# Performance work log

Measured on AMD Instinct MI355X. Metric: run time of the kernel, lower is better.

## Reference

```python
import jax, jax.numpy as jnp
import numpy as np

N_LOW, N_HIGH = 20000, 60000
E_LOW, E_L2H, E_HIGH = 320000, 540000, 480000
EPS = 1e-5
NEG_SLOPE = 0.2


def _gatv2(x_src, x_dst, edge_index, Wl, Wr, att, bias):
    """PyG GATv2Conv with concat heads, aggr='mean', no self loops.
    att: [H, C]. Returns [n_dst, H*C]."""
    H, C = att.shape
    n_dst = x_dst.shape[0]
    xl = (x_src @ Wl).reshape(-1, H, C)   # [n_src, H, C]
    xr = (x_dst @ Wr).reshape(-1, H, C)   # [n_dst, H, C]
    src, dst = edge_index[0], edge_index[1]
    z = jax.nn.leaky_relu(xl[src] + xr[dst], NEG_SLOPE)        # [E, H, C]
    logits = jnp.einsum('ehc,hc->eh', z, att)                  # [E, H]
    m = jax.ops.segment_max(logits, dst, num_segments=n_dst)   # segment softmax
    e = jnp.exp(logits - m[dst])
    s = jax.ops.segment_sum(e, dst, num_segments=n_dst)
    alpha = e / s[dst]                                         # [E, H]
    out = jax.ops.segment_sum(xl[src] * alpha[:, :, None], dst, num_segments=n_dst)
    deg = jax.ops.segment_sum(jnp.ones((src.shape[0],), out.dtype), dst, num_segments=n_dst)
    out = out / jnp.maximum(deg, 1.0)[:, None, None]           # aggr='mean'
    out = out.reshape(n_dst, H * C)
    if bias is not None:
        out = out + bias
    return out


def _bn(x, g, b):
    mu = x.mean(axis=0)
    var = x.var(axis=0)
    return (x - mu) * jax.lax.rsqrt(var + EPS) * g + b


def _forward(x_low, x_high, z_std, e_low, e_l2h, e_high,
             l1_Wl, l1_Wr, l1_att, l1_b, bn1_g, bn1_b,
             l2_Wl, l2_Wr, l2_att, l2_b, bn2_g, bn2_b,
             l3_Wl, l3_Wr, l3_att, l3_b,
             lh_Wl, lh_Wr, lh_att,
             h1_Wl, h1_Wr, h1_att, h1_b, bn3_g, bn3_b,
             h2_Wl, h2_Wr, h2_att, h2_b, bn4_g, bn4_b,
             h3_Wl, h3_Wr, h3_att, h3_b):
    # low_net: GATv2(125->128,h2) -> BN(256) -> GATv2(256->128) -> BN(128) -> GATv2(128->128)
    h = _gatv2(x_low, x_low, e_low, l1_Wl, l1_Wr, l1_att, l1_b)
    h = _bn(h, bn1_g, bn1_b)
    h = _gatv2(h, h, e_low, l2_Wl, l2_Wr, l2_att, l2_b)
    h = _bn(h, bn2_g, bn2_b)
    h = _gatv2(h, h, e_low, l3_Wl, l3_Wr, l3_att, l3_b)
    # bipartite low2high: (encod_low[128], x_high[1]) -> 128, no bias
    eh = _gatv2(h, x_high, e_l2h, lh_Wl, lh_Wr, lh_att, None)
    eh = jnp.concatenate([z_std, eh], axis=-1)                 # [N_HIGH, 129]
    # high_net
    g = _gatv2(eh, eh, e_high, h1_Wl, h1_Wr, h1_att, h1_b)
    g = _bn(g, bn3_g, bn3_b)
    g = _gatv2(g, g, e_high, h2_Wl, h2_Wr, h2_att, h2_b)
    g = _bn(g, bn4_g, bn4_b)
    return _gatv2(g, g, e_high, h3_Wl, h3_Wr, h3_att, h3_b)   # [N_HIGH, 2]


def setup_inputs() -> dict:
    key = jax.random.key(0)
    ks = iter(jax.random.split(key, 64))
    def P(shape, fan_in):
        return jax.random.normal(next(ks), shape, jnp.float32) / np.sqrt(fan_in)
    inp = {}
    inp['x_low'] = jax.random.normal(next(ks), (N_LOW, 125), jnp.float32)
    inp['x_high'] = jax.random.normal(next(ks), (N_HIGH, 1), jnp.float32)
    inp['z_std'] = jax.random.normal(next(ks), (N_HIGH, 1), jnp.float32)
    inp['e_low'] = jnp.stack([jax.random.randint(next(ks), (E_LOW,), 0, N_LOW),
                              jax.random.randint(next(ks), (E_LOW,), 0, N_LOW)])
    inp['e_l2h'] = jnp.stack([jax.random.randint(next(ks), (E_L2H,), 0, N_LOW),
                              jax.random.randint(next(ks), (E_L2H,), 0, N_HIGH)])
    inp['e_high'] = jnp.stack([jax.random.randint(next(ks), (E_HIGH,), 0, N_HIGH),
                               jax.random.randint(next(ks), (E_HIGH,), 0, N_HIGH)])
    inp['l1_Wl'] = P((125, 256), 125); inp['l1_Wr'] = P((125, 256), 125)
    inp['l1_att'] = P((2, 128), 128);  inp['l1_b'] = jnp.zeros((256,), jnp.float32)
    inp['bn1_g'] = jnp.ones((256,), jnp.float32); inp['bn1_b'] = jnp.zeros((256,), jnp.float32)
    inp['l2_Wl'] = P((256, 128), 256); inp['l2_Wr'] = P((256, 128), 256)
    inp['l2_att'] = P((1, 128), 128);  inp['l2_b'] = jnp.zeros((128,), jnp.float32)
    inp['bn2_g'] = jnp.ones((128,), jnp.float32); inp['bn2_b'] = jnp.zeros((128,), jnp.float32)
    inp['l3_Wl'] = P((128, 128), 128); inp['l3_Wr'] = P((128, 128), 128)
    inp['l3_att'] = P((1, 128), 128);  inp['l3_b'] = jnp.zeros((128,), jnp.float32)
    inp['lh_Wl'] = P((128, 128), 128); inp['lh_Wr'] = P((1, 128), 1)
    inp['lh_att'] = P((1, 128), 128)
    inp['h1_Wl'] = P((129, 256), 129); inp['h1_Wr'] = P((129, 256), 129)
    inp['h1_att'] = P((2, 128), 128);  inp['h1_b'] = jnp.zeros((256,), jnp.float32)
    inp['bn3_g'] = jnp.ones((256,), jnp.float32); inp['bn3_b'] = jnp.zeros((256,), jnp.float32)
    inp['h2_Wl'] = P((256, 128), 256); inp['h2_Wr'] = P((256, 128), 256)
    inp['h2_att'] = P((1, 128), 128);  inp['h2_b'] = jnp.zeros((128,), jnp.float32)
    inp['bn4_g'] = jnp.ones((128,), jnp.float32); inp['bn4_b'] = jnp.zeros((128,), jnp.float32)
    inp['h3_Wl'] = P((128, 2), 128);   inp['h3_Wr'] = P((128, 2), 128)
    inp['h3_att'] = P((1, 2), 2);      inp['h3_b'] = jnp.zeros((2,), jnp.float32)
    return inp


def reference(x_low, x_high, z_std, e_low, e_l2h, e_high,
              l1_Wl, l1_Wr, l1_att, l1_b, bn1_g, bn1_b,
              l2_Wl, l2_Wr, l2_att, l2_b, bn2_g, bn2_b,
              l3_Wl, l3_Wr, l3_att, l3_b,
              lh_Wl, lh_Wr, lh_att,
              h1_Wl, h1_Wr, h1_att, h1_b, bn3_g, bn3_b,
              h2_Wl, h2_Wr, h2_att, h2_b, bn4_g, bn4_b,
              h3_Wl, h3_Wr, h3_att, h3_b):
    return _forward(x_low, x_high, z_std, e_low, e_l2h, e_high,
                    l1_Wl, l1_Wr, l1_att, l1_b, bn1_g, bn1_b,
                    l2_Wl, l2_Wr, l2_att, l2_b, bn2_g, bn2_b,
                    l3_Wl, l3_Wr, l3_att, l3_b,
                    lh_Wl, lh_Wr, lh_att,
                    h1_Wl, h1_Wr, h1_att, h1_b, bn3_g, bn3_b,
                    h2_Wl, h2_Wr, h2_att, h2_b, bn4_g, bn4_b,
                    h3_Wl, h3_Wr, h3_att, h3_b)
```

## Files before the change

kernel.cpp:

```cpp
#include <hip/hip_runtime.h>
#include <hip/hip_bf16.h>
#include <cstdint>
#include <cstddef>
#include <cmath>

#define NEG_SLOPE 0.2f

#define PB  1024
#define CSH 10
#define CBS 1024
#define NBCMAX 160
#define PBN 2048

using frag = __attribute__((ext_vector_type(8))) short;
using facc = __attribute__((ext_vector_type(4))) float;

__device__ __forceinline__ float bf_hi(unsigned u) {
    union { unsigned i; float f; } t; t.i = u & 0xffff0000u; return t.f;
}
__device__ __forceinline__ float bf_lo(unsigned u) {
    union { unsigned i; float f; } t; t.i = u << 16; return t.f;
}
__device__ __forceinline__ void unpack8(uint4 u, float* v) {
    v[0] = bf_lo(u.x); v[1] = bf_hi(u.x);
    v[2] = bf_lo(u.y); v[3] = bf_hi(u.y);
    v[4] = bf_lo(u.z); v[5] = bf_hi(u.z);
    v[6] = bf_lo(u.w); v[7] = bf_hi(u.w);
}

typedef const __attribute__((address_space(1))) void* gas_cptr;
typedef __attribute__((address_space(3))) void* las_ptr;
__device__ __forceinline__ void gload_lds16(const __hip_bfloat16* g, __hip_bfloat16* l) {
    __builtin_amdgcn_global_load_lds((gas_cptr)(const void*)g, (las_ptr)(void*)l, 16, 0, 0);
}

__global__ __launch_bounds__(256)
void msplitA(const int* __restrict__ s0, const int* __restrict__ d0, int E0,
             const int* __restrict__ s1, const int* __restrict__ d1, int E1,
             const int* __restrict__ s2, const int* __restrict__ d2, int E2,
             int nc0, int nc1, int nc2, int cap0, int cap1, int cap2,
             int* __restrict__ stage, int* __restrict__ cnt2) {
    __shared__ int hist[NBCMAX];
    __shared__ int rbase[NBCMAX];
    __shared__ int curs[NBCMAX];
    __shared__ int ord[1024];
    __shared__ int obkt[1024];
    const int NBC = nc0 + nc1 + nc2;
    const long Etot = (long)E0 + E1 + E2;
    int tid = threadIdx.x;
    int lane = tid & 63;
    long chunk = (Etot + PB - 1) / PB;
    long c0 = (long)blockIdx.x * chunk;
    long c1 = c0 + chunk; if (c1 > Etot) c1 = Etot;
    const long sec1 = (long)PB * nc0 * cap0;
    const long sec2 = sec1 + (long)PB * nc1 * cap1;
    for (int t = tid; t < NBC; t += 256) curs[t] = 0;
    __syncthreads();
    for (long r0 = c0; r0 < c1; r0 += 1024) {
        int n = (int)((c1 - r0 < 1024) ? (c1 - r0) : 1024);
        for (int t = tid; t < NBC; t += 256) hist[t] = 0;
        __syncthreads();
        int mye[4], myb[4], myr[4];
#pragma unroll
        for (int k = 0; k < 4; ++k) {
            int li = k * 256 + tid;
            myb[k] = -1;
            if (li < n) {
                long i = r0 + li;
                int src, dst, gb;
                if (i < E0) { src = s0[i]; dst = d0[i]; gb = dst >> CSH; }
                else if (i < (long)E0 + E1) { long j = i - E0; src = s1[j]; dst = d1[j]; gb = nc0 + (dst >> CSH); }
                else { long j = i - E0 - E1; src = s2[j]; dst = d2[j]; gb = nc0 + nc1 + (dst >> CSH); }
                mye[k] = (src << CSH) | (dst & (CBS - 1));
                myb[k] = gb;
                myr[k] = atomicAdd(&hist[gb], 1);
            }
        }
        __syncthreads();
        if (tid < 64) {
            int carry = 0;
            for (int base = 0; base < NBC; base += 64) {
                int g = base + lane;
                int v = (g < NBC) ? hist[g] : 0;
                int sum = v;
#pragma unroll
                for (int o = 1; o < 64; o <<= 1) {
                    int t = __shfl_up(sum, o, 64);
                    if (lane >= o) sum += t;
                }
                if (g < NBC) rbase[g] = carry + sum - v;
                carry += __shfl(sum, 63, 64);
            }
        }
        __syncthreads();
#pragma unroll
        for (int k = 0; k < 4; ++k)
            if (myb[k] >= 0) {
                int pos = rbase[myb[k]] + myr[k];
                ord[pos] = mye[k];
                obkt[pos] = myb[k];
            }
        __syncthreads();
        for (int pos = tid; pos < n; pos += 256) {
            int b = obkt[pos];
            int rank = pos - rbase[b] + curs[b];
            long addr; int cap;
            if (b < nc0)            { cap = cap0; addr = (long)(blockIdx.x * nc0 + b) * cap0; }
            else if (b < nc0 + nc1) { cap = cap1; addr = sec1 + (long)(blockIdx.x * nc1 + (b - nc0)) * cap1; }
            else                    { cap = cap2; addr = sec2 + (long)(blockIdx.x * nc2 + (b - nc0 - nc1)) * cap2; }
            if (rank < cap) stage[addr + rank] = ord[pos];
        }
        __syncthreads();
        for (int t = tid; t < NBC; t += 256) curs[t] += hist[t];
        __syncthreads();
    }
    for (int t = tid; t < NBC; t += 256) {
        int cap = (t < nc0) ? cap0 : (t < nc0 + nc1) ? cap1 : cap2;
        int c = curs[t]; if (c > cap) c = cap;
        cnt2[(long)blockIdx.x * NBC + t] = c;
    }
}

__global__ void scanC1(const int* __restrict__ cnt2, int* __restrict__ tot, int NBC) {
    __shared__ int red[256];
    int gb = blockIdx.x;
    int tid = threadIdx.x;
    int s = 0;
    for (int p = tid; p < PB; p += 256) s += cnt2[(long)p * NBC + gb];
    red[tid] = s;
    __syncthreads();
    for (int o = 128; o; o >>= 1) {
        if (tid < o) red[tid] += red[tid + o];
        __syncthreads();
    }
    if (tid == 0) tot[gb] = red[0];
}

__global__ void scanC2(const int* __restrict__ tot, int* __restrict__ cstart,
                       int NBC, int nc0, int nc1) {
    if (threadIdx.x == 0) {
        int c = 0;
        for (int gb = 0; gb < NBC; ++gb) {
            if (gb == nc0 || gb == nc0 + nc1) c = 0;
            cstart[gb] = c;
            c += tot[gb];
        }
    }
}

__global__ __launch_bounds__(1024)
void fineB(const int* __restrict__ cnt2, const int* __restrict__ cstart,
           const int* __restrict__ stage,
           int nc0, int nc1, int nc2, int cap0, int cap1, int cap2,
           int* __restrict__ off0, int* __restrict__ col0, int n0,
           int* __restrict__ off1, int* __restrict__ col1, int n1,
           int* __restrict__ off2, int* __restrict__ col2, int n2) {
    __shared__ int fragb[PB + 1];
    __shared__ int cnt[1024];
    __shared__ int wsum[17];
    const int NBC = nc0 + nc1 + nc2;
    int gb = blockIdx.x;
    int tid = threadIdx.x;
    int lane = tid & 63;
    int wv = tid >> 6;
    int cb, ncg, n; long base2, stride; int* off; int* col;
    const long sec1 = (long)PB * nc0 * cap0;
    const long sec2 = sec1 + (long)PB * nc1 * cap1;
    if (gb < nc0) {
        cb = gb; ncg = nc0; n = n0; off = off0; col = col0;
        base2 = (long)cb * cap0; stride = (long)nc0 * cap0;
    } else if (gb < nc0 + nc1) {
        cb = gb - nc0; ncg = nc1; n = n1; off = off1; col = col1;
        base2 = sec1 + (long)cb * cap1; stride = (long)nc1 * cap1;
    } else {
        cb = gb - nc0 - nc1; ncg = nc2; n = n2; off = off2; col = col2;
        base2 = sec2 + (long)cb * cap2; stride = (long)nc2 * cap2;
    }
    int dlo = cb << CSH;
    int colbase = cstart[gb];
    int v = cnt2[(long)tid * NBC + gb];
    int sum = v;
#pragma unroll
    for (int o = 1; o < 64; o <<= 1) {
        int t = __shfl_up(sum, o, 64);
        if (lane >= o) sum += t;
    }
    if (lane == 63) wsum[wv] = sum;
    __syncthreads();
    if (tid == 0) {
        int c = 0;
        for (int w = 0; w < 16; ++w) { int t = wsum[w]; wsum[w] = c; c += t; }
        wsum[16] = c;
    }
    __syncthreads();
    fragb[tid] = wsum[wv] + sum - v;
    if (tid == 0) fragb[PB] = wsum[16];
    __syncthreads();
    int sz = fragb[PB];
    cnt[tid] = 0;
    __syncthreads();
    for (int p = tid; p < sz; p += 1024) {
        int lo = 0, hi = PB;
        while (hi - lo > 1) { int mid = (lo + hi) >> 1; if (fragb[mid] <= p) lo = mid; else hi = mid; }
        int e = stage[base2 + (long)lo * stride + (p - fragb[lo])];
        atomicAdd(&cnt[e & (CBS - 1)], 1);
    }
    __syncthreads();
    int cv = cnt[tid];
    int csum = cv;
#pragma unroll
    for (int o = 1; o < 64; o <<= 1) {
        int t = __shfl_up(csum, o, 64);
        if (lane >= o) csum += t;
    }
    if (lane == 63) wsum[wv] = csum;
    __syncthreads();
    if (tid == 0) {
        int c = 0;
        for (int w = 0; w < 16; ++w) { int t = wsum[w]; wsum[w] = c; c += t; }
    }
    __syncthreads();
    int excl = wsum[wv] + csum - cv;
    int d = dlo + tid;
    if (d < n) off[d] = colbase + excl;
    if (cb == ncg - 1 && tid == 0) off[n] = colbase + sz;
    __syncthreads();
    cnt[tid] = colbase + excl;
    __syncthreads();
    for (int p = tid; p < sz; p += 1024) {
        int lo = 0, hi = PB;
        while (hi - lo > 1) { int mid = (lo + hi) >> 1; if (fragb[mid] <= p) lo = mid; else hi = mid; }
        int e = stage[base2 + (long)lo * stride + (p - fragb[lo])];
        int pos = atomicAdd(&cnt[e & (CBS - 1)], 1);
        col[pos] = e >> CSH;
    }
}

__global__ __launch_bounds__(256)
void gemm_bf16_mfma(const __hip_bfloat16* __restrict__ A,
                    const __hip_bfloat16* __restrict__ Bt,
                    __hip_bfloat16* __restrict__ C,
                    const float* __restrict__ bias, int M, int N, int Kp) {
    __shared__ __hip_bfloat16 As[128 * 32];
    __shared__ __hip_bfloat16 Bs[128 * 32];
    int tid = threadIdx.x;
    int lane = tid & 63;
    int wave = tid >> 6;
    int wm = wave >> 1, wn = wave & 1;
    int quad = lane >> 4, l16 = lane & 15;
    int m0 = blockIdx.y * 128;
    int n0 = blockIdx.x * 128;

    facc acc[4][4] = {};

    for (int k0 = 0; k0 < Kp; k0 += 32) {
#pragma unroll
        for (int p = 0; p < 2; ++p) {
            int idx = p * 256 + tid;
            int row = idx >> 2;
            int koff = (idx & 3) * 8;
            int gr = m0 + row; if (gr >= M) gr = M - 1;
            int lbase = (p * 256 + wave * 64) * 8;
            gload_lds16(A + (size_t)gr * Kp + k0 + koff, As + lbase);
            gload_lds16(Bt + (size_t)(n0 + row) * Kp + k0 + koff, Bs + lbase);
        }
        __syncthreads();

        frag a[4], b[4];
#pragma unroll
        for (int i = 0; i < 4; ++i) {
            a[i] = *reinterpret_cast<const frag*>(As + (wm * 64 + i * 16 + l16) * 32 + quad * 8);
            b[i] = *reinterpret_cast<const frag*>(Bs + (wn * 64 + i * 16 + l16) * 32 + quad * 8);
        }
#pragma unroll
        for (int i = 0; i < 4; ++i)
#pragma unroll
            for (int j = 0; j < 4; ++j)
                acc[i][j] = __builtin_amdgcn_mfma_f32_16x16x32_bf16(a[i], b[j], acc[i][j], 0, 0, 0);
        __syncthreads();
    }

#pragma unroll
    for (int i = 0; i < 4; ++i)
#pragma unroll
        for (int j = 0; j < 4; ++j) {
            int col = n0 + wn * 64 + j * 16 + l16;
            float bv = (bias != nullptr) ? bias[col] : 0.f;
#pragma unroll
            for (int r = 0; r < 4; ++r) {
                int row = m0 + wm * 64 + i * 16 + quad * 4 + r;
                if (row < M) C[(size_t)row * N + col] = __float2bfloat16(acc[i][j][r] + bv);
            }
        }
}

__global__ void gemm_n22_bn(const __hip_bfloat16* __restrict__ A,
                            const float* __restrict__ Wl, const float* __restrict__ Wr,
                            const float* __restrict__ s, const float* __restrict__ t,
                            float* __restrict__ YL, float* __restrict__ YR, int M, int K) {
    int i = blockIdx.x * blockDim.x + threadIdx.x;
    if (i >= M) return;
    float l0 = 0.f, l1 = 0.f, r0 = 0.f, r1 = 0.f;
    const unsigned* a = (const unsigned*)(A + (size_t)i * K);
    for (int k2 = 0; k2 < K / 2; ++k2) {
        unsigned u = a[k2];
        int k = k2 * 2;
        float v0 = fmaf(bf_lo(u), s[k], t[k]);
        float v1 = fmaf(bf_hi(u), s[k + 1], t[k + 1]);
        l0 = fmaf(v0, Wl[k * 2 + 0], l0);
        l1 = fmaf(v0, Wl[k * 2 + 1], l1);
        l0 = fmaf(v1, Wl[k * 2 + 2], l0);
        l1 = fmaf(v1, Wl[k * 2 + 3], l1);
        r0 = fmaf(v0, Wr[k * 2 + 0], r0);
        r1 = fmaf(v0, Wr[k * 2 + 1], r1);
        r0 = fmaf(v1, Wr[k * 2 + 2], r0);
        r1 = fmaf(v1, Wr[k * 2 + 3], r1);
    }
    YL[(size_t)i * 2 + 0] = l0;
    YL[(size_t)i * 2 + 1] = l1;
    YR[(size_t)i * 2 + 0] = r0;
    YR[(size_t)i * 2 + 1] = r1;
}

__global__ void prep_all(const float* __restrict__ l1Wl, const float* __restrict__ l1Wr,
                         const float* __restrict__ lhWl,
                         const float* __restrict__ h1Wl, const float* __restrict__ h1Wr,
                         const float* __restrict__ x_low, const float* __restrict__ x_high,
                         const float* __restrict__ lhWr, const float* __restrict__ z_std,
                         __hip_bfloat16* __restrict__ w_l1, __hip_bfloat16* __restrict__ w_lh,
                         __hip_bfloat16* __restrict__ w_h1,
                         __hip_bfloat16* __restrict__ XLOWB, __hip_bfloat16* __restrict__ XRo,
                         __hip_bfloat16* __restrict__ EHB,
                         int o1, int o2, int o3, int o4, int o5, int o6, int o7, int o8) {
    int i = blockIdx.x * blockDim.x + threadIdx.x;
    if (i < o1) {
        int r = i >> 7, c = i & 127;
        XLOWB[i] = __float2bfloat16((c < 125) ? x_low[(size_t)r * 125 + c] : 0.f);
    } else if (i < o2) {
        int j = i - o1; int r = j >> 7, c = j & 127;
        XRo[j] = __float2bfloat16(x_high[r] * lhWr[c]);
    } else if (i < o3) {
        int j = i - o2; int r = j >> 5, c = (j & 31) + 128;
        EHB[(size_t)r * 160 + c] = __float2bfloat16((c == 128) ? z_std[r] : 0.f);
    } else if (i < o4) {
        int j = i - o3; int n = j >> 7, k = j & 127;
        w_l1[j] = __float2bfloat16((k < 125) ? l1Wl[(size_t)k * 256 + n] : 0.f);
    } else if (i < o5) {
        int j = i - o4; int n = j >> 7, k = j & 127;
        w_l1[256 * 128 + j] = __float2bfloat16((k < 125) ? l1Wr[(size_t)k * 256 + n] : 0.f);
    } else if (i < o6) {
        int j = i - o5; int n = j >> 7, k = j & 127;
        w_lh[j] = __float2bfloat16(lhWl[(size_t)k * 128 + n]);
    } else if (i < o7) {
        int j = i - o6; int n = j / 160, k = j - n * 160;
        float v = 0.f;
        if (k < 128) v = h1Wl[(size_t)(k + 1) * 256 + n];
        else if (k == 128) v = h1Wl[n];
        w_h1[j] = __float2bfloat16(v);
    } else if (i < o8) {
        int j = i - o7; int n = j / 160, k = j - n * 160;
        float v = 0.f;
        if (k < 128) v = h1Wr[(size_t)(k + 1) * 256 + n];
        else if (k == 128) v = h1Wr[n];
        w_h1[256 * 160 + j] = __float2bfloat16(v);
    }
}

__global__ void wconv_bnfold2(const float* __restrict__ Wl, const float* __restrict__ Wr,
                              const float* __restrict__ scale, const float* __restrict__ shift,
                              __hip_bfloat16* __restrict__ Wt, float* __restrict__ bout,
                              int K, int N, int Kp) {
    __shared__ float red[256];
    const float* W = blockIdx.y ? Wr : Wl;
    __hip_bfloat16* wt = Wt + (size_t)blockIdx.y * N * Kp;
    float* bo = bout + blockIdx.y * N;
    int n = blockIdx.x;
    int tid = threadIdx.x;
    float acc = 0.f;
    for (int k = tid; k < Kp; k += 256) {
        float v = 0.f;
        if (k < K) {
            float w = W[(size_t)k * N + n];
            v = w * scale[k];
            acc = fmaf(w, shift[k], acc);
        }
        wt[(size_t)n * Kp + k] = __float2bfloat16(v);
    }
    red[tid] = acc;
    __syncthreads();
    for (int o = 128; o; o >>= 1) {
        if (tid < o) red[tid] += red[tid + o];
        __syncthreads();
    }
    if (tid == 0) bo[n] = red[0];
}

__global__ void gat_c128_v4(const __hip_bfloat16* __restrict__ xl, int xls,
                            const __hip_bfloat16* __restrict__ xr, int xrs,
                            const int* __restrict__ row_off, const int* __restrict__ col,
                            const float* __restrict__ att, const float* __restrict__ bias,
                            __hip_bfloat16* __restrict__ outb, int obstride,
                            int n_dst, int H) {
    int wid = (blockIdx.x * blockDim.x + threadIdx.x) >> 6;
    int lane = threadIdx.x & 63;
    int total = n_dst * H;
    if (wid >= total) return;
    int dst = wid / H;
    int h = wid - dst * H;
    int g = lane >> 4;
    int q = lane & 15;
    int cb = h * 128 + q * 8;
    int beg = row_off[dst], end = row_off[dst + 1];

    float xrv[8], av[8];
    unpack8(*(const uint4*)(xr + (size_t)dst * xrs + cb), xrv);
    {
        float4 a0 = *(const float4*)(att + cb);
        float4 a1 = *(const float4*)(att + cb + 4);
        av[0] = a0.x; av[1] = a0.y; av[2] = a0.z; av[3] = a0.w;
        av[4] = a1.x; av[5] = a1.y; av[6] = a1.z; av[7] = a1.w;
    }

    float s = 0.f;
    float acc[8] = {0.f, 0.f, 0.f, 0.f, 0.f, 0.f, 0.f, 0.f};

    if (beg < end) {
        int e0g = beg + g;
        bool pv = e0g < end;
        int i0 = col[pv ? e0g : beg];
        uint4 u = *(const uint4*)(xl + (size_t)i0 * xls + cb);
        int e1g = beg + 4 + g;
        int i1 = (beg + 4 < end) ? col[(e1g < end) ? e1g : beg] : 0;

        for (int e0 = beg; e0 < end; e0 += 4) {
            bool have_next = (e0 + 4) < end;
            uint4 un;
            if (have_next)
                un = *(const uint4*)(xl + (size_t)i1 * xls + cb);
            int e2g = e0 + 8 + g;
            int i2 = (e0 + 8 < end) ? col[(e2g < end) ? e2g : beg] : 0;
            bool nv = (e0 + 4 + g) < end;

            float v[8];
            unpack8(u, v);
            float p = 0.f;
#pragma unroll
            for (int c = 0; c < 8; ++c) {
                float z = v[c] + xrv[c];
                z = fmaxf(z, NEG_SLOPE * z);
                p = fmaf(z, av[c], p);
            }
            p += __shfl_xor(p, 8, 64);
            p += __shfl_xor(p, 4, 64);
            p += __shfl_xor(p, 2, 64);
            p += __shfl_xor(p, 1, 64);
            if (!pv) p = -INFINITY;
            float w = __expf(fminf(p, 85.f));
            s += w;
#pragma unroll
            for (int c = 0; c < 8; ++c) acc[c] = fmaf(w, v[c], acc[c]);

            if (have_next) { u = un; pv = nv; }
            i1 = i2;
        }
    }

#pragma unroll
    for (int o = 16; o <= 32; o <<= 1) {
        s += __shfl_xor(s, o, 64);
#pragma unroll
        for (int c = 0; c < 8; ++c) acc[c] += __shfl_xor(acc[c], o, 64);
    }

    int deg = end - beg;
    float inv = (deg > 0) ? 1.f / (s * (float)deg) : 0.f;
    float o8[8];
#pragma unroll
    for (int c = 0; c < 8; ++c) o8[c] = acc[c] * inv;
    if (bias != nullptr) {
#pragma unroll
        for (int c = 0; c < 8; ++c) o8[c] += bias[cb + c];
    }
    if (g == 0) {
        union { uint4 u; __hip_bfloat16 hh[8]; } pk;
#pragma unroll
        for (int c = 0; c < 8; ++c) pk.hh[c] = __float2bfloat16(o8[c]);
        *(uint4*)(outb + (size_t)dst * obstride + cb) = pk.u;
    }
}

__global__ void gat_c256h2(const __hip_bfloat16* __restrict__ xl, int xls,
                           const __hip_bfloat16* __restrict__ xr, int xrs,
                           const int* __restrict__ row_off, const int* __restrict__ col,
                           const float* __restrict__ att, const float* __restrict__ bias,
                           __hip_bfloat16* __restrict__ outb, int obstride,
                           int n_dst) {
    int dst = (blockIdx.x * blockDim.x + threadIdx.x) >> 6;
    int lane = threadIdx.x & 63;
    if (dst >= n_dst) return;
    int g = lane >> 5;
    int q = lane & 31;
    int cb = q * 8;
    int beg = row_off[dst], end = row_off[dst + 1];

    float xrv[8], av[8];
    unpack8(*(const uint4*)(xr + (size_t)dst * xrs + cb), xrv);
    {
        float4 a0 = *(const float4*)(att + cb);
        float4 a1 = *(const float4*)(att + cb + 4);
        av[0] = a0.x; av[1] = a0.y; av[2] = a0.z; av[3] = a0.w;
        av[4] = a1.x; av[5] = a1.y; av[6] = a1.z; av[7] = a1.w;
    }

    float s = 0.f;
    float acc[8] = {0.f, 0.f, 0.f, 0.f, 0.f, 0.f, 0.f, 0.f};

    if (beg < end) {
        int e0g = beg + g;
        bool pv = e0g < end;
        int i0 = col[pv ? e0g : beg];
        uint4 u = *(const uint4*)(xl + (size_t)i0 * xls + cb);
        int e1g = beg + 2 + g;
        int i1 = (beg + 2 < end) ? col[(e1g < end) ? e1g : beg] : 0;

        for (int e0 = beg; e0 < end; e0 += 2) {
            bool have_next = (e0 + 2) < end;
            uint4 un;
            if (have_next)
                un = *(const uint4*)(xl + (size_t)i1 * xls + cb);
            int e2g = e0 + 4 + g;
            int i2 = (e0 + 4 < end) ? col[(e2g < end) ? e2g : beg] : 0;
            bool nv = (e0 + 2 + g) < end;

            float v[8];
            unpack8(u, v);
            float p = 0.f;
#pragma unroll
            for (int c = 0; c < 8; ++c) {
                float z = v[c] + xrv[c];
                z = fmaxf(z, NEG_SLOPE * z);
                p = fmaf(z, av[c], p);
            }
            p += __shfl_xor(p, 8, 64);
            p += __shfl_xor(p, 4, 64);
            p += __shfl_xor(p, 2, 64);
            p += __shfl_xor(p, 1, 64);
            if (!pv) p = -INFINITY;
            float w = __expf(fminf(p, 85.f));
            s += w;
#pragma unroll
            for (int c = 0; c < 8; ++c) acc[c] = fmaf(w, v[c], acc[c]);

            if (have_next) { u = un; pv = nv; }
            i1 = i2;
        }
    }

    s += __shfl_xor(s, 32, 64);
#pragma unroll
    for (int c = 0; c < 8; ++c) acc[c] += __shfl_xor(acc[c], 32, 64);

    int deg = end - beg;
    float inv = (deg > 0) ? 1.f / (s * (float)deg) : 0.f;
    float o8[8];
#pragma unroll
    for (int c = 0; c < 8; ++c) o8[c] = acc[c] * inv;
    if (bias != nullptr) {
#pragma unroll
        for (int c = 0; c < 8; ++c) o8[c] += bias[cb + c];
    }
    if (g == 0) {
        union { uint4 u; __hip_bfloat16 hh[8]; } pk;
#pragma unroll
        for (int c = 0; c < 8; ++c) pk.hh[c] = __float2bfloat16(o8[c]);
        *(uint4*)(outb + (size_t)dst * obstride + cb) = pk.u;
    }
}

__global__ void gat_c2(const float* __restrict__ xl, const float* __restrict__ xr,
                       const int* __restrict__ row_off, const int* __restrict__ col,
                       const float* __restrict__ att, const float* __restrict__ bias,
                       float* __restrict__ out, int n_dst) {
    int dst = blockIdx.x * blockDim.x + threadIdx.x;
    if (dst >= n_dst) return;
    float x0 = xr[(size_t)dst * 2], x1 = xr[(size_t)dst * 2 + 1];
    float a0 = att[0], a1 = att[1];
    int beg = row_off[dst], end = row_off[dst + 1];
    float s = 0.f, acc0 = 0.f, acc1 = 0.f;
    for (int e = beg; e < end; ++e) {
        int src = col[e];
        float v0 = xl[(size_t)src * 2], v1 = xl[(size_t)src * 2 + 1];
        float z0 = v0 + x0; z0 = fmaxf(z0, NEG_SLOPE * z0);
        float z1 = v1 + x1; z1 = fmaxf(z1, NEG_SLOPE * z1);
        float p = fmaf(z0, a0, z1 * a1);
        float w = __expf(fminf(p, 85.f));
        s += w;
        acc0 = fmaf(w, v0, acc0);
        acc1 = fmaf(w, v1, acc1);
    }
    int deg = end - beg;
    float o0 = 0.f, o1 = 0.f;
    if (deg > 0) {
        float inv = 1.f / (s * (float)deg);
        o0 = acc0 * inv;
        o1 = acc1 * inv;
    }
    out[(size_t)dst * 2 + 0] = o0 + bias[0];
    out[(size_t)dst * 2 + 1] = o1 + bias[1];
}

__global__ void bn_partial_d(const __hip_bfloat16* __restrict__ x, float* __restrict__ part,
                             int Nr, int rpb) {
    int C = blockDim.x;
    int c = threadIdx.x;
    int b = blockIdx.x;
    int r0 = b * rpb;
    int r1 = r0 + rpb; if (r1 > Nr) r1 = Nr;
    float s = 0.f, q = 0.f;
    for (int r = r0; r < r1; ++r) {
        float v = __bfloat162float(x[(size_t)r * C + c]);
        s += v;
        q = fmaf(v, v, q);
    }
    part[(size_t)b * C + c] = s;
    part[(size_t)PBN * 256 + (size_t)b * C + c] = q;
}

__global__ void bn_finalize_w(const float* __restrict__ part,
                              const float* __restrict__ g, const float* __restrict__ b,
                              float* __restrict__ scale, float* __restrict__ shift,
                              int Nr, int C) {
    int c = (blockIdx.x * blockDim.x + threadIdx.x) >> 6;
    int lane = threadIdx.x & 63;
    if (c >= C) return;
    float s = 0.f, q = 0.f;
    for (int blk = lane; blk < PBN; blk += 64) {
        s += part[(size_t)blk * C + c];
        q += part[(size_t)PBN * 256 + (size_t)blk * C + c];
    }
#pragma unroll
    for (int o = 32; o; o >>= 1) {
        s += __shfl_xor(s, o, 64);
        q += __shfl_xor(q, o, 64);
    }
    if (lane == 0) {
        float mu = s / (float)Nr;
        float var = q / (float)Nr - mu * mu;
        float inv = rsqrtf(var + 1e-5f);
        float a = g[c] * inv;
        scale[c] = a;
        shift[c] = b[c] - mu * a;
    }
}

extern "C" void kernel_launch(void* const* d_in, const int* in_sizes, int n_in,
                              void* d_out, int out_size, void* d_ws, size_t ws_size,
                              hipStream_t stream) {
    const float* x_low  = (const float*)d_in[0];
    const float* x_high = (const float*)d_in[1];
    const float* z_std  = (const float*)d_in[2];
    const int* e_low  = (const int*)d_in[3];
    const int* e_l2h  = (const int*)d_in[4];
    const int* e_high = (const int*)d_in[5];
    const float* l1_Wl = (const float*)d_in[6];
    const float* l1_Wr = (const float*)d_in[7];
    const float* l1_att = (const float*)d_in[8];
    const float* l1_b  = (const float*)d_in[9];
    const float* bn1_g = (const float*)d_in[10];
    const float* bn1_b = (const float*)d_in[11];
    const float* l2_Wl = (const float*)d_in[12];
    const float* l2_Wr = (const float*)d_in[13];
    const float* l2_att = (const float*)d_in[14];
    const float* l2_b  = (const float*)d_in[15];
    const float* bn2_g = (const float*)d_in[16];
    const float* bn2_b = (const float*)d_in[17];
    const float* l3_Wl = (const float*)d_in[18];
    const float* l3_Wr = (const float*)d_in[19];
    const float* l3_att = (const float*)d_in[20];
    const float* l3_b  = (const float*)d_in[21];
    const float* lh_Wl = (const float*)d_in[22];
    const float* lh_Wr = (const float*)d_in[23];
    const float* lh_att = (const float*)d_in[24];
    const float* h1_Wl = (const float*)d_in[25];
    const float* h1_Wr = (const float*)d_in[26];
    const float* h1_att = (const float*)d_in[27];
    const float* h1_b  = (const float*)d_in[28];
    const float* bn3_g = (const float*)d_in[29];
    const float* bn3_b = (const float*)d_in[30];
    const float* h2_Wl = (const float*)d_in[31];
    const float* h2_Wr = (const float*)d_in[32];
    const float* h2_att = (const float*)d_in[33];
    const float* h2_b  = (const float*)d_in[34];
    const float* bn4_g = (const float*)d_in[35];
    const float* bn4_b = (const float*)d_in[36];
    const float* h3_Wl = (const float*)d_in[37];
    const float* h3_Wr = (const float*)d_in[38];
    const float* h3_att = (const float*)d_in[39];
    const float* h3_b  = (const float*)d_in[40];

    const int N_low = in_sizes[0] / 125;
    const int N_high = in_sizes[1];
    const int E_low = in_sizes[3] / 2;
    const int E_l2h = in_sizes[4] / 2;
    const int E_high = in_sizes[5] / 2;

    char* ws = (char*)d_ws;
    size_t woff = 0;
    auto walloc = [&](size_t bytes) -> void* {
        void* p = (void*)(ws + woff);
        woff += (bytes + 255) & ~(size_t)255;
        return p;
    };
    __hip_bfloat16* XLR = (__hip_bfloat16*)walloc((size_t)N_high * 512 * 2);
    __hip_bfloat16* A1  = (__hip_bfloat16*)walloc((size_t)N_high * 256 * 2);
    __hip_bfloat16* A2  = (__hip_bfloat16*)walloc((size_t)N_high * 128 * 2);
    __hip_bfloat16* XRo = (__hip_bfloat16*)walloc((size_t)N_high * 128 * 2);
    __hip_bfloat16* XLOWB = (__hip_bfloat16*)walloc((size_t)N_low * 128 * 2);
    __hip_bfloat16* EHB = (__hip_bfloat16*)walloc((size_t)N_high * 160 * 2);
    float* YL = (float*)walloc((size_t)N_high * 2 * 4);
    float* YR = (float*)walloc((size_t)N_high * 2 * 4);
    int* off_low  = (int*)walloc((size_t)(N_low + 1) * 4);
    int* col_low  = (int*)walloc((size_t)E_low * 4);
    int* off_l2h  = (int*)walloc((size_t)(N_high + 1) * 4);
    int* col_l2h  = (int*)walloc((size_t)E_l2h * 4);
    int* off_high = (int*)walloc((size_t)(N_high + 1) * 4);
    int* col_high = (int*)walloc((size_t)E_high * 4);
    const int nc0 = (N_low + CBS - 1) >> CSH;
    const int nc1 = (N_high + CBS - 1) >> CSH;
    const int nc2 = (N_high + CBS - 1) >> CSH;
    const int NBC = nc0 + nc1 + nc2;
    const long Etot = (long)E_low + E_l2h + E_high;
    const long chunk = (Etot + PB - 1) / PB;
    auto capf = [&](int ng) {
        double m = (double)chunk * CBS / ng;
        int c = (int)(m + 8.0 * sqrt(m) + 16.0);
        return (c + 15) & ~15;
    };
    const int cap0 = capf(N_low);
    const int cap1 = capf(N_high);
    const int cap2 = capf(N_high);
    int* cnt2   = (int*)walloc((size_t)PB * NBC * 4);
    int* cstart = (int*)walloc((size_t)(NBC + 1) * 4);
    int* ctot   = (int*)walloc((size_t)(NBC + 1) * 4);
    float* bnpart = (float*)walloc((size_t)2 * PBN * 256 * 4);
    float* bnsc   = (float*)walloc(512 * 4);
    float* bb     = (float*)walloc(512 * 4);
    __hip_bfloat16* w_l1 = (__hip_bfloat16*)walloc(512 * 128 * 2);
    __hip_bfloat16* w_l2 = (__hip_bfloat16*)walloc(256 * 256 * 2);
    __hip_bfloat16* w_l3 = (__hip_bfloat16*)walloc(256 * 128 * 2);
    __hip_bfloat16* w_lh = (__hip_bfloat16*)walloc(128 * 128 * 2);
    __hip_bfloat16* w_h1 = (__hip_bfloat16*)walloc(512 * 160 * 2);
    __hip_bfloat16* w_h2 = (__hip_bfloat16*)walloc(256 * 256 * 2);

    int* stage = (int*)XLR;

    {
        int o1 = N_low * 128;
        int o2 = o1 + N_high * 128;
        int o3 = o2 + N_high * 32;
        int o4 = o3 + 256 * 128;
        int o5 = o4 + 256 * 128;
        int o6 = o5 + 128 * 128;
        int o7 = o6 + 256 * 160;
        int o8 = o7 + 256 * 160;
        prep_all<<<(o8 + 255) / 256, 256, 0, stream>>>(
            l1_Wl, l1_Wr, lh_Wl, h1_Wl, h1_Wr, x_low, x_high, lh_Wr, z_std,
            w_l1, w_lh, w_h1, XLOWB, XRo, EHB,
            o1, o2, o3, o4, o5, o6, o7, o8);
    }

    msplitA<<<PB, 256, 0, stream>>>(
        e_low, e_low + E_low, E_low,
        e_l2h, e_l2h + E_l2h, E_l2h,
        e_high, e_high + E_high, E_high,
        nc0, nc1, nc2, cap0, cap1, cap2, stage, cnt2);
    scanC1<<<NBC, 256, 0, stream>>>(cnt2, ctot, NBC);
    scanC2<<<1, 64, 0, stream>>>(ctot, cstart, NBC, nc0, nc1);
    fineB<<<NBC, 1024, 0, stream>>>(cnt2, cstart, stage,
                                    nc0, nc1, nc2, cap0, cap1, cap2,
                                    off_low, col_low, N_low,
                                    off_l2h, col_l2h, N_high,
                                    off_high, col_high, N_high);

    auto gemm = [&](const __hip_bfloat16* A, const __hip_bfloat16* Bt, __hip_bfloat16* C,
                    int M, int N, int Kp, const float* bias) {
        dim3 g(N / 128, (M + 127) / 128);
        gemm_bf16_mfma<<<g, 256, 0, stream>>>(A, Bt, C, bias, M, N, Kp);
    };
    auto gat1 = [&](const __hip_bfloat16* xl, int xls, const __hip_bfloat16* xr, int xrs,
                    const int* roff, const int* colv,
                    const float* att, const float* bias,
                    __hip_bfloat16* outb, int obs, int n_dst) {
        long thr = (long)n_dst * 64;
        gat_c128_v4<<<(unsigned)((thr + 255) / 256), 256, 0, stream>>>(
            xl, xls, xr, xrs, roff, colv, att, bias, outb, obs, n_dst, 1);
    };
    auto gat2 = [&](const __hip_bfloat16* xl, int xls, const __hip_bfloat16* xr, int xrs,
                    const int* roff, const int* colv,
                    const float* att, const float* bias,
                    __hip_bfloat16* outb, int obs, int n_dst) {
        long thr = (long)n_dst * 64;
        gat_c256h2<<<(unsigned)((thr + 255) / 256), 256, 0, stream>>>(
            xl, xls, xr, xrs, roff, colv, att, bias, outb, obs, n_dst);
    };
    auto bn_stats = [&](__hip_bfloat16* x, const float* g, const float* b, int Nr, int C) {
        int rpb = (Nr + PBN - 1) / PBN;
        bn_partial_d<<<PBN, C, 0, stream>>>(x, bnpart, Nr, rpb);
        bn_finalize_w<<<(C * 64 + 255) / 256, 256, 0, stream>>>(bnpart, g, b, bnsc, bnsc + 256, Nr, C);
    };
    auto fold2 = [&](const float* Wl, const float* Wr, __hip_bfloat16* Wt,
                     int K, int Nn, int Kp) {
        dim3 g(Nn, 2);
        wconv_bnfold2<<<g, 256, 0, stream>>>(Wl, Wr, bnsc, bnsc + 256, Wt, bb, K, Nn, Kp);
    };

    gemm(XLOWB, w_l1, XLR, N_low, 512, 128, nullptr);
    gat2(XLR, 512, XLR + 256, 512, off_low, col_low, l1_att, l1_b, A1, 256, N_low);
    bn_stats(A1, bn1_g, bn1_b, N_low, 256);

    fold2(l2_Wl, l2_Wr, w_l2, 256, 128, 256);
    gemm(A1, w_l2, XLR, N_low, 256, 256, bb);
    gat1(XLR, 256, XLR + 128, 256, off_low, col_low, l2_att, l2_b, A2, 128, N_low);
    bn_stats(A2, bn2_g, bn2_b, N_low, 128);

    fold2(l3_Wl, l3_Wr, w_l3, 128, 128, 128);
    gemm(A2, w_l3, XLR, N_low, 256, 128, bb);
    gat1(XLR, 256, XLR + 128, 256, off_low, col_low, l3_att, l3_b, A1, 128, N_low);

    gemm(A1, w_lh, XLR, N_low, 128, 128, nullptr);
    gat1(XLR, 128, XRo, 128, off_l2h, col_l2h, lh_att, nullptr, EHB, 160, N_high);

    gemm(EHB, w_h1, XLR, N_high, 512, 160, nullptr);
    gat2(XLR, 512, XLR + 256, 512, off_high, col_high, h1_att, h1_b, A1, 256, N_high);
    bn_stats(A1, bn3_g, bn3_b, N_high, 256);

    fold2(h2_Wl, h2_Wr, w_h2, 256, 128, 256);
    gemm(A1, w_h2, XLR, N_high, 256, 256, bb);
    gat1(XLR, 256, XLR + 128, 256, off_high, col_high, h2_att, h2_b, A2, 128, N_high);
    bn_stats(A2, bn4_g, bn4_b, N_high, 128);

    gemm_n22_bn<<<(N_high + 255) / 256, 256, 0, stream>>>(A2, h3_Wl, h3_Wr,
                                                          bnsc, bnsc + 256, YL, YR, N_high, 128);
    gat_c2<<<(N_high + 255) / 256, 256, 0, stream>>>(YL, YR, off_high, col_high,
                                                     h3_att, h3_b, (float*)d_out, N_high);
}
```

Baseline: 657.0 us.

## Template bf16 MFMA GEMM on K with large K-steps and vectorized stores

Makes the GEMM a template over the padded K and the K-step, so a whole 128 or 160 K slice is staged in LDS per barrier instead of 32 at a time. Swaps the MFMA operands so each lane holds four consecutive output columns, allowing packed 8-byte bf16 stores and float4 bias loads. The aim is fewer synchronisations and loop iterations and wider global writes. The cost is a larger LDS footprint per block, which may lower occupancy, and K must match one of the specialised sizes.

```diff
diff --git a/kernel.cpp b/kernel.cpp
--- a/kernel.cpp
+++ b/kernel.cpp
@@ -236,13 +236,16 @@
     }
 }
 
+template<int KP, int KSTEP>
 __global__ __launch_bounds__(256)
-void gemm_bf16_mfma(const __hip_bfloat16* __restrict__ A,
-                    const __hip_bfloat16* __restrict__ Bt,
-                    __hip_bfloat16* __restrict__ C,
-                    const float* __restrict__ bias, int M, int N, int Kp) {
-    __shared__ __hip_bfloat16 As[128 * 32];
-    __shared__ __hip_bfloat16 Bs[128 * 32];
+void gemm_t(const __hip_bfloat16* __restrict__ A,
+            const __hip_bfloat16* __restrict__ Bt,
+            __hip_bfloat16* __restrict__ C,
+            const float* __restrict__ bias, int M, int N) {
+    constexpr int CPR = KSTEP / 8;
+    constexpr int ITER = CPR / 2;
+    __shared__ __hip_bfloat16 As[128 * KSTEP];
+    __shared__ __hip_bfloat16 Bs[128 * KSTEP];
     int tid = threadIdx.x;
     int lane = tid & 63;
     int wave = tid >> 6;
@@ -253,45 +256,57 @@
 
     facc acc[4][4] = {};
 
-    for (int k0 = 0; k0 < Kp; k0 += 32) {
-#pragma unroll
-        for (int p = 0; p < 2; ++p) {
+    for (int k0 = 0; k0 < KP; k0 += KSTEP) {
+        if (k0) __syncthreads();
+#pragma unroll
+        for (int p = 0; p < ITER; ++p) {
             int idx = p * 256 + tid;
-            int row = idx >> 2;
-            int koff = (idx & 3) * 8;
+            int row = idx / CPR;
+            int c = idx - row * CPR;
             int gr = m0 + row; if (gr >= M) gr = M - 1;
             int lbase = (p * 256 + wave * 64) * 8;
-            gload_lds16(A + (size_t)gr * Kp + k0 + koff, As + lbase);
-            gload_lds16(Bt + (size_t)(n0 + row) * Kp + k0 + koff, Bs + lbase);
+            gload_lds16(A + (size_t)gr * KP + k0 + c * 8, As + lbase);
+            gload_lds16(Bt + (size_t)(n0 + row) * KP + k0 + c * 8, Bs + lbase);
         }
         __syncthreads();
-
-        frag a[4], b[4];
-#pragma unroll
-        for (int i = 0; i < 4; ++i) {
-            a[i] = *reinterpret_cast<const frag*>(As + (wm * 64 + i * 16 + l16) * 32 + quad * 8);
-            b[i] = *reinterpret_cast<const frag*>(Bs + (wn * 64 + i * 16 + l16) * 32 + quad * 8);
-        }
-#pragma unroll
-        for (int i = 0; i < 4; ++i)
-#pragma unroll
-            for (int j = 0; j < 4; ++j)
-                acc[i][j] = __builtin_amdgcn_mfma_f32_16x16x32_bf16(a[i], b[j], acc[i][j], 0, 0, 0);
-        __syncthreads();
-    }
-
-#pragma unroll
-    for (int i = 0; i < 4; ++i)
+#pragma unroll
+        for (int kk = 0; kk < KSTEP / 32; ++kk) {
+            frag a[4], b[4];
+#pragma unroll
+            for (int i = 0; i < 4; ++i) {
+                a[i] = *(const frag*)(As + (wm * 64 + i * 16 + l16) * KSTEP + kk * 32 + quad * 8);
+                b[i] = *(const frag*)(Bs + (wn * 64 + i * 16 + l16) * KSTEP + kk * 32 + quad * 8);
+            }
+#pragma unroll
+            for (int i = 0; i < 4; ++i)
+#pragma unroll
+                for (int j = 0; j < 4; ++j)
+                    acc[i][j] = __builtin_amdgcn_mfma_f32_16x16x32_bf16(b[j], a[i], acc[i][j], 0, 0, 0);
+        }
+    }
+
+    float4 bv[4];
+#pragma unroll
+    for (int j = 0; j < 4; ++j) {
+        int n = n0 + wn * 64 + j * 16 + quad * 4;
+        if (bias != nullptr) bv[j] = *(const float4*)(bias + n);
+        else { bv[j].x = 0.f; bv[j].y = 0.f; bv[j].z = 0.f; bv[j].w = 0.f; }
+    }
+#pragma unroll
+    for (int i = 0; i < 4; ++i) {
+        int m = m0 + wm * 64 + i * 16 + l16;
+        if (m >= M) continue;
 #pragma unroll
         for (int j = 0; j < 4; ++j) {
-            int col = n0 + wn * 64 + j * 16 + l16;
-            float bv = (bias != nullptr) ? bias[col] : 0.f;
-#pragma unroll
-            for (int r = 0; r < 4; ++r) {
-                int row = m0 + wm * 64 + i * 16 + quad * 4 + r;
-                if (row < M) C[(size_t)row * N + col] = __float2bfloat16(acc[i][j][r] + bv);
-            }
-        }
+            int n = n0 + wn * 64 + j * 16 + quad * 4;
+            union { uint2 u; __hip_bfloat16 hh[4]; } pk;
+            pk.hh[0] = __float2bfloat16(acc[i][j][0] + bv[j].x);
+            pk.hh[1] = __float2bfloat16(acc[i][j][1] + bv[j].y);
+            pk.hh[2] = __float2bfloat16(acc[i][j][2] + bv[j].z);
+            pk.hh[3] = __float2bfloat16(acc[i][j][3] + bv[j].w);
+            *(uint2*)(C + (size_t)m * N + n) = pk.u;
+        }
+    }
 }
 
 __global__ void gemm_n22_bn(const __hip_bfloat16* __restrict__ A,
@@ -785,7 +800,9 @@
     auto gemm = [&](const __hip_bfloat16* A, const __hip_bfloat16* Bt, __hip_bfloat16* C,
                     int M, int N, int Kp, const float* bias) {
         dim3 g(N / 128, (M + 127) / 128);
-        gemm_bf16_mfma<<<g, 256, 0, stream>>>(A, Bt, C, bias, M, N, Kp);
+        if (Kp == 128)      gemm_t<128, 128><<<g, 256, 0, stream>>>(A, Bt, C, bias, M, N);
+        else if (Kp == 160) gemm_t<160, 160><<<g, 256, 0, stream>>>(A, Bt, C, bias, M, N);
+        else                gemm_t<256, 128><<<g, 256, 0, stream>>>(A, Bt, C, bias, M, N);
     };
     auto gat1 = [&](const __hip_bfloat16* xl, int xls, const __hip_bfloat16* xr, int xrs,
                     const int* roff, const int* colv,
```

Result: faster. 611.7 us (-6.9%).
